# Performance work log

Hardware: AMD Instinct MI355X
Metric: run time of the kernel (lower is better)

## Reference

```python
import jax, jax.numpy as jnp
import numpy as np

DIM = 1024
HIDDEN = 2048
NUM_EXPERTS = 8
TOP_K = 2


def setup_inputs() -> dict:
    key = jax.random.key(0)
    ks = jax.random.split(key, 5)
    x = jax.random.normal(ks[0], (4, 1024, DIM), dtype=jnp.float32)
    # router: torch Linear(dim, num_experts, bias=False) -> store as [dim, E]
    Wr = jax.random.normal(ks[1], (DIM, NUM_EXPERTS), dtype=jnp.float32) * 0.02
    # stacked expert weights (SwiGLU): w1/w3 [E, dim, hidden], w2 [E, hidden, dim]
    W1 = jax.random.normal(ks[2], (NUM_EXPERTS, DIM, HIDDEN), dtype=jnp.float32) * 0.02
    W3 = jax.random.normal(ks[3], (NUM_EXPERTS, DIM, HIDDEN), dtype=jnp.float32) * 0.02
    W2 = jax.random.normal(ks[4], (NUM_EXPERTS, HIDDEN, DIM), dtype=jnp.float32) * 0.02
    return {"x": x, "Wr": Wr, "W1": W1, "W2": W2, "W3": W3}


def reference(x, Wr, W1, W2, W3):
    B, S, D = x.shape
    T = B * S
    xf = x.reshape(T, D)
    # router: softmax over experts, then top-k and renormalize
    probs = jax.nn.softmax(xf @ Wr, axis=-1)                  # [T, E]
    topk_p, topk_i = jax.lax.top_k(probs, TOP_K)              # [T, K]
    topk_p = topk_p / jnp.sum(topk_p, axis=-1, keepdims=True)
    # per-(token, expert) combine weight; zero for non-selected experts
    gate = jnp.sum(jax.nn.one_hot(topk_i, NUM_EXPERTS, dtype=xf.dtype)
                   * topk_p[:, :, None], axis=1)              # [T, E]
    # SwiGLU experts, computed densely then masked-combined (same math as
    # the masked dispatch loop: out[t] = sum_e gate[t,e] * expert_e(x[t]))
    h = jax.nn.silu(jnp.einsum('td,edh->teh', xf, W1)) \
        * jnp.einsum('td,edh->teh', xf, W3)                   # [T, E, H]
    out_e = jnp.einsum('teh,ehd->ted', h, W2)                 # [T, E, D]
    out = jnp.einsum('ted,te->td', out_e, gate)               # [T, D]
    return out.reshape(B, S, D)
```

## Files before the change

### kernel.cpp

```cpp
#include <hip/hip_runtime.h>
#include <hip/hip_bf16.h>
#include <stdint.h>

#define T_TOK 4096
#define DIM   1024
#define HID   2048
#define NE    8

typedef unsigned short ushort_t;
typedef __attribute__((ext_vector_type(8))) short bf16x8;
typedef __attribute__((ext_vector_type(4))) float f32x4;

__device__ __forceinline__ unsigned short f2bf(float f) {
  unsigned u = __float_as_uint(f);
  unsigned r = (u + 0x7fffu + ((u >> 16) & 1u)) >> 16;
  return (unsigned short)r;
}

__device__ __forceinline__ void gl2lds16(const ushort_t* g, ushort_t* l) {
  void* gv = (void*)g;
  __builtin_amdgcn_global_load_lds((__attribute__((address_space(1))) void*)gv,
                                   (__attribute__((address_space(3))) void*)l,
                                   16, 0, 0);
}

__global__ __launch_bounds__(256)
void prep_kernel(const float* __restrict__ x, const float* __restrict__ Wr,
                 const float* __restrict__ W1, const float* __restrict__ W2,
                 const float* __restrict__ W3,
                 ushort_t* __restrict__ xb,
                 ushort_t* __restrict__ w1t, ushort_t* __restrict__ w3t,
                 ushort_t* __restrict__ w2t,
                 int* __restrict__ cnt, int* __restrict__ tok,
                 float* __restrict__ gate, float* __restrict__ out) {
  const int b = blockIdx.x;
  const int tid = threadIdx.x;
  __shared__ float lds[64][65];

  if (b < 12288) {
    const float* src; ushort_t* dst; int R, C, cx, ry;
    const int which = b >> 12;
    const int id = b & 4095;
    const int e = id >> 9, rem = id & 511;
    if (which == 0)      { src = W1; dst = w1t; R = DIM; C = HID; cx = rem & 31; ry = rem >> 5; }
    else if (which == 1) { src = W3; dst = w3t; R = DIM; C = HID; cx = rem & 31; ry = rem >> 5; }
    else                 { src = W2; dst = w2t; R = HID; C = DIM; cx = rem & 15; ry = rem >> 4; }
    const float* s = src + (size_t)e * R * C;
    ushort_t* d = dst + (size_t)e * R * C;
    const int c0 = cx * 64, r0 = ry * 64;
#pragma unroll
    for (int p = 0; p < 4; p++) {
      int idx = p * 256 + tid;
      int r = idx >> 4, c4 = idx & 15;
      float4 v = *(const float4*)(s + (size_t)(r0 + r) * C + c0 + c4 * 4);
      lds[r][c4 * 4 + 0] = v.x; lds[r][c4 * 4 + 1] = v.y;
      lds[r][c4 * 4 + 2] = v.z; lds[r][c4 * 4 + 3] = v.w;
    }
    __syncthreads();
#pragma unroll
    for (int p = 0; p < 4; p++) {
      int idx = p * 256 + tid;
      int cc = idx >> 4, r4 = idx & 15;
      ushort4 o;
      o.x = f2bf(lds[r4 * 4 + 0][cc]);
      o.y = f2bf(lds[r4 * 4 + 1][cc]);
      o.z = f2bf(lds[r4 * 4 + 2][cc]);
      o.w = f2bf(lds[r4 * 4 + 3][cc]);
      *(ushort4*)(d + (size_t)(c0 + cc) * R + r0 + r4 * 4) = o;
    }
  } else if (b < 16384) {
    int i = (b - 12288) * 256 + tid;
    float4 v = ((const float4*)x)[i];
    ushort4 o;
    o.x = f2bf(v.x); o.y = f2bf(v.y); o.z = f2bf(v.z); o.w = f2bf(v.w);
    ((ushort4*)xb)[i] = o;
  } else if (b < 17408) {
    const int wave = tid >> 6;
    const int lane = tid & 63;
    const int t = (b - 16384) * 4 + wave;
    float acc[NE];
#pragma unroll
    for (int e = 0; e < NE; e++) acc[e] = 0.f;
    const float* xr = x + (size_t)t * DIM;
    for (int dd = lane; dd < DIM; dd += 64) {
      float xv = xr[dd];
      const float* wr = Wr + (size_t)dd * NE;
#pragma unroll
      for (int e = 0; e < NE; e++) acc[e] += xv * wr[e];
    }
#pragma unroll
    for (int off = 32; off >= 1; off >>= 1) {
#pragma unroll
      for (int e = 0; e < NE; e++) acc[e] += __shfl_xor(acc[e], off, 64);
    }
    if (lane == 0) {
      int i1 = 0;
#pragma unroll
      for (int e = 1; e < NE; e++) if (acc[e] > acc[i1]) i1 = e;
      int i2 = (i1 == 0) ? 1 : 0;
#pragma unroll
      for (int e = 0; e < NE; e++) {
        if (e == i1) continue;
        if (acc[e] > acc[i2]) i2 = e;
      }
      float r = expf(acc[i2] - acc[i1]);
      float g1 = 1.f / (1.f + r);
      float g2 = 1.f - g1;
      int p;
      p = atomicAdd(&cnt[i1], 1); tok[i1 * T_TOK + p] = t; gate[i1 * T_TOK + p] = g1;
      p = atomicAdd(&cnt[i2], 1); tok[i2 * T_TOK + p] = t; gate[i2 * T_TOK + p] = g2;
    }
  } else {
    int base_i = (b - 17408) * 1024;
    float4 z = {0.f, 0.f, 0.f, 0.f};
#pragma unroll
    for (int it = 0; it < 4; it++) ((float4*)out)[base_i + it * 256 + tid] = z;
  }
}

__global__ __launch_bounds__(256, 3)
void gemm1_kernel(const ushort_t* __restrict__ xb,
                  const ushort_t* __restrict__ w1t,
                  const ushort_t* __restrict__ w3t,
                  const int* __restrict__ tok,
                  const float* __restrict__ gates,
                  const int* __restrict__ cnt,
                  ushort_t* __restrict__ hbuf) {
  const int e = blockIdx.z, mt = blockIdx.y, nt = blockIdx.x;
  const int Ne = cnt[e];
  if (mt * 128 >= Ne) return;
  int be = 0;
#pragma unroll
  for (int i = 0; i < NE; i++) be += (i < e) ? cnt[i] : 0;

  __shared__ __attribute__((aligned(16))) ushort_t lA[128 * 64];
  __shared__ __attribute__((aligned(16))) ushort_t lB1[64 * 64];
  __shared__ __attribute__((aligned(16))) ushort_t lB3[64 * 64];

  const int tid = threadIdx.x, lane = tid & 63, wave = tid >> 6;
  const int kco = ((tid & 7) ^ ((tid >> 3) & 7)) * 8;

  const ushort_t* pA[4];
#pragma unroll
  for (int it = 0; it < 4; it++) {
    int rowg = mt * 128 + it * 32 + (tid >> 3);
    int t = (rowg < Ne) ? tok[e * T_TOK + rowg] : 0;
    pA[it] = xb + (size_t)t * DIM + kco;
  }
  const int h0 = nt * 64;
  const ushort_t* pB1[2];
  const ushort_t* pB3[2];
#pragma unroll
  for (int it = 0; it < 2; it++) {
    int row = h0 + it * 32 + (tid >> 3);
    pB1[it] = w1t + ((size_t)e * HID + row) * DIM + kco;
    pB3[it] = w3t + ((size_t)e * HID + row) * DIM + kco;
  }

  f32x4 c1[4][2], c3[4][2];
#pragma unroll
  for (int i = 0; i < 4; i++)
#pragma unroll
    for (int j = 0; j < 2; j++) {
      c1[i][j] = (f32x4){0.f, 0.f, 0.f, 0.f};
      c3[i][j] = (f32x4){0.f, 0.f, 0.f, 0.f};
    }

  const int wm = (wave >> 1) * 64, wn = (wave & 1) * 32;
  const int m = lane & 15, kq = lane >> 4;
  int aRow[4], bRow[2], cSlot[2];
#pragma unroll
  for (int i = 0; i < 4; i++) aRow[i] = (wm + i * 16 + m) * 64;
#pragma unroll
  for (int j = 0; j < 2; j++) bRow[j] = (wn + j * 16 + m) * 64;
#pragma unroll
  for (int u = 0; u < 2; u++) cSlot[u] = ((u * 4 + kq) ^ (m & 7)) * 8;

  for (int k0 = 0; k0 < DIM; k0 += 64) {
#pragma unroll
    for (int it = 0; it < 4; it++) gl2lds16(pA[it] + k0, lA + (it * 256 + tid) * 8);
#pragma unroll
    for (int it = 0; it < 2; it++) {
      gl2lds16(pB1[it] + k0, lB1 + (it * 256 + tid) * 8);
      gl2lds16(pB3[it] + k0, lB3 + (it * 256 + tid) * 8);
    }
    __syncthreads();
#pragma unroll
    for (int u = 0; u < 2; u++) {
      bf16x8 a[4], b1f[2], b3f[2];
#pragma unroll
      for (int i = 0; i < 4; i++) a[i] = *(const bf16x8*)(lA + aRow[i] + cSlot[u]);
#pragma unroll
      for (int j = 0; j < 2; j++) {
        b1f[j] = *(const bf16x8*)(lB1 + bRow[j] + cSlot[u]);
        b3f[j] = *(const bf16x8*)(lB3 + bRow[j] + cSlot[u]);
      }
#pragma unroll
      for (int i = 0; i < 4; i++)
#pragma unroll
        for (int j = 0; j < 2; j++) {
          c1[i][j] = __builtin_amdgcn_mfma_f32_16x16x32_bf16(a[i], b1f[j], c1[i][j], 0, 0, 0);
          c3[i][j] = __builtin_amdgcn_mfma_f32_16x16x32_bf16(a[i], b3f[j], c3[i][j], 0, 0, 0);
        }
    }
    __syncthreads();
  }

  const int m4 = lane >> 4;
#pragma unroll
  for (int i = 0; i < 4; i++) {
#pragma unroll
    for (int j = 0; j < 2; j++) {
      int hcol = h0 + wn + j * 16 + m;
#pragma unroll
      for (int reg = 0; reg < 4; reg++) {
        int rowg = mt * 128 + wm + i * 16 + m4 * 4 + reg;
        if (rowg < Ne) {
          float v1 = c1[i][j][reg];
          float v3 = c3[i][j][reg];
          float g = gates[e * T_TOK + rowg];
          float hv = g * (v1 / (1.f + expf(-v1))) * v3;
          hbuf[(size_t)(be + rowg) * HID + hcol] = f2bf(hv);
        }
      }
    }
  }
}

__global__ __launch_bounds__(256, 3)
void gemm2_kernel(const ushort_t* __restrict__ hbuf,
                  const ushort_t* __restrict__ w2t,
                  const int* __restrict__ tok,
                  const int* __restrict__ cnt,
                  float* __restrict__ out) {
  const int e = blockIdx.z, mt = blockIdx.y, nt = blockIdx.x;
  const int Ne = cnt[e];
  if (mt * 128 >= Ne) return;
  int be = 0;
#pragma unroll
  for (int i = 0; i < NE; i++) be += (i < e) ? cnt[i] : 0;

  __shared__ __attribute__((aligned(16))) ushort_t lA[128 * 64];
  __shared__ __attribute__((aligned(16))) ushort_t lB[128 * 64];

  const int tid = threadIdx.x, lane = tid & 63, wave = tid >> 6;
  const int kco = ((tid & 7) ^ ((tid >> 3) & 7)) * 8;

  const ushort_t* pA[4];
#pragma unroll
  for (int it = 0; it < 4; it++) {
    int rr = min(mt * 128 + it * 32 + (tid >> 3), Ne - 1);
    pA[it] = hbuf + (size_t)(be + rr) * HID + kco;
  }
  const int d0 = nt * 128;
  const ushort_t* pB[4];
#pragma unroll
  for (int it = 0; it < 4; it++) {
    int row = d0 + it * 32 + (tid >> 3);
    pB[it] = w2t + ((size_t)e * DIM + row) * HID + kco;
  }

  f32x4 c[4][4];
#pragma unroll
  for (int i = 0; i < 4; i++)
#pragma unroll
    for (int j = 0; j < 4; j++) c[i][j] = (f32x4){0.f, 0.f, 0.f, 0.f};

  const int wm = (wave >> 1) * 64, wn = (wave & 1) * 64;
  const int m = lane & 15, kq = lane >> 4;
  int aRow[4], bRow[4], cSlot[2];
#pragma unroll
  for (int i = 0; i < 4; i++) aRow[i] = (wm + i * 16 + m) * 64;
#pragma unroll
  for (int j = 0; j < 4; j++) bRow[j] = (wn + j * 16 + m) * 64;
#pragma unroll
  for (int u = 0; u < 2; u++) cSlot[u] = ((u * 4 + kq) ^ (m & 7)) * 8;

  for (int k0 = 0; k0 < HID; k0 += 64) {
#pragma unroll
    for (int it = 0; it < 4; it++) {
      gl2lds16(pA[it] + k0, lA + (it * 256 + tid) * 8);
      gl2lds16(pB[it] + k0, lB + (it * 256 + tid) * 8);
    }
    __syncthreads();
#pragma unroll
    for (int u = 0; u < 2; u++) {
      bf16x8 a[4], bf[4];
#pragma unroll
      for (int i = 0; i < 4; i++) a[i] = *(const bf16x8*)(lA + aRow[i] + cSlot[u]);
#pragma unroll
      for (int j = 0; j < 4; j++) bf[j] = *(const bf16x8*)(lB + bRow[j] + cSlot[u]);
#pragma unroll
      for (int i = 0; i < 4; i++)
#pragma unroll
        for (int j = 0; j < 4; j++)
          c[i][j] = __builtin_amdgcn_mfma_f32_16x16x32_bf16(a[i], bf[j], c[i][j], 0, 0, 0);
    }
    __syncthreads();
  }

  const int m4 = lane >> 4;
#pragma unroll
  for (int i = 0; i < 4; i++) {
    int rowg = mt * 128 + wm + i * 16 + m4 * 4;
    if (rowg >= Ne) continue;
#pragma unroll
    for (int reg = 0; reg < 4; reg++) {
      int rg = rowg + reg;
      if (rg < Ne) {
        int t = tok[e * T_TOK + rg];
        float* orow = out + (size_t)t * DIM;
#pragma unroll
        for (int j = 0; j < 4; j++) {
          int dcol = d0 + wn + j * 16 + m;
          atomicAdd(orow + dcol, c[i][j][reg]);
        }
      }
    }
  }
}

extern "C" void kernel_launch(void* const* d_in, const int* in_sizes, int n_in,
                              void* d_out, int out_size, void* d_ws, size_t ws_size,
                              hipStream_t stream) {
  (void)in_sizes; (void)n_in; (void)ws_size; (void)out_size;
  const float* x  = (const float*)d_in[0];
  const float* Wr = (const float*)d_in[1];
  const float* W1 = (const float*)d_in[2];
  const float* W2 = (const float*)d_in[3];
  const float* W3 = (const float*)d_in[4];
  float* out = (float*)d_out;

  char* w = (char*)d_ws;
  ushort_t* xb   = (ushort_t*)w; w += (size_t)T_TOK * DIM * 2;
  ushort_t* w1t  = (ushort_t*)w; w += (size_t)NE * DIM * HID * 2;
  ushort_t* w3t  = (ushort_t*)w; w += (size_t)NE * DIM * HID * 2;
  ushort_t* w2t  = (ushort_t*)w; w += (size_t)NE * HID * DIM * 2;
  ushort_t* hbuf = (ushort_t*)w; w += (size_t)2 * T_TOK * HID * 2;
  int*   tok   = (int*)w;   w += (size_t)NE * T_TOK * 4;
  float* gates = (float*)w; w += (size_t)NE * T_TOK * 4;
  int*   cnt   = (int*)w;   w += 128;

  hipMemsetAsync(cnt, 0, 128, stream);
  prep_kernel<<<18432, 256, 0, stream>>>(x, Wr, W1, W2, W3, xb, w1t, w3t, w2t,
                                         cnt, tok, gates, out);
  gemm1_kernel<<<dim3(HID / 64, 32, NE), 256, 0, stream>>>(xb, w1t, w3t, tok, gates, cnt, hbuf);
  gemm2_kernel<<<dim3(DIM / 128, 32, NE), 256, 0, stream>>>(hbuf, w2t, tok, cnt, out);
}
```

Measured before the change: 485.6 us.

## Fuse bf16 cast of x into router pass and move expert dispatch to compact kernel

The router blocks now read each token row once as float4, writing the bf16 copy of x and accumulating the router logits in the same loop. This removes the separate cast-blocks pass over x. Per-token expert ids and gate pairs are stored, and a new single-block compact kernel builds the per-expert token lists using LDS atomics instead of global atomics. That also drops the hipMemsetAsync, but adds an extra serial kernel launch with only one workgroup.

```diff
diff --git a/kernel.cpp b/kernel.cpp
--- a/kernel.cpp
+++ b/kernel.cpp
@@ -31,8 +31,8 @@
                  ushort_t* __restrict__ xb,
                  ushort_t* __restrict__ w1t, ushort_t* __restrict__ w3t,
                  ushort_t* __restrict__ w2t,
-                 int* __restrict__ cnt, int* __restrict__ tok,
-                 float* __restrict__ gate, float* __restrict__ out) {
+                 int* __restrict__ eidx, float2* __restrict__ gpair,
+                 float* __restrict__ out) {
   const int b = blockIdx.x;
   const int tid = threadIdx.x;
   __shared__ float lds[64][65];
@@ -68,25 +68,28 @@
       o.w = f2bf(lds[r4 * 4 + 3][cc]);
       *(ushort4*)(d + (size_t)(c0 + cc) * R + r0 + r4 * 4) = o;
     }
-  } else if (b < 16384) {
-    int i = (b - 12288) * 256 + tid;
-    float4 v = ((const float4*)x)[i];
-    ushort4 o;
-    o.x = f2bf(v.x); o.y = f2bf(v.y); o.z = f2bf(v.z); o.w = f2bf(v.w);
-    ((ushort4*)xb)[i] = o;
-  } else if (b < 17408) {
+  } else if (b < 13312) {
     const int wave = tid >> 6;
     const int lane = tid & 63;
-    const int t = (b - 16384) * 4 + wave;
+    const int t = (b - 12288) * 4 + wave;
+    const float* xr = x + (size_t)t * DIM;
+    ushort_t* xbr = xb + (size_t)t * DIM;
     float acc[NE];
 #pragma unroll
     for (int e = 0; e < NE; e++) acc[e] = 0.f;
-    const float* xr = x + (size_t)t * DIM;
-    for (int dd = lane; dd < DIM; dd += 64) {
-      float xv = xr[dd];
-      const float* wr = Wr + (size_t)dd * NE;
-#pragma unroll
-      for (int e = 0; e < NE; e++) acc[e] += xv * wr[e];
+#pragma unroll
+    for (int it = 0; it < 4; it++) {
+      int d4 = it * 64 + lane;
+      float4 v = ((const float4*)xr)[d4];
+      ushort4 o;
+      o.x = f2bf(v.x); o.y = f2bf(v.y); o.z = f2bf(v.z); o.w = f2bf(v.w);
+      ((ushort4*)xbr)[d4] = o;
+      const float* wr = Wr + (size_t)d4 * 4 * NE;
+      float c[4] = {v.x, v.y, v.z, v.w};
+#pragma unroll
+      for (int cc = 0; cc < 4; cc++)
+#pragma unroll
+        for (int e = 0; e < NE; e++) acc[e] += c[cc] * wr[cc * NE + e];
     }
 #pragma unroll
     for (int off = 32; off >= 1; off >>= 1) {
@@ -105,17 +108,36 @@
       }
       float r = expf(acc[i2] - acc[i1]);
       float g1 = 1.f / (1.f + r);
-      float g2 = 1.f - g1;
-      int p;
-      p = atomicAdd(&cnt[i1], 1); tok[i1 * T_TOK + p] = t; gate[i1 * T_TOK + p] = g1;
-      p = atomicAdd(&cnt[i2], 1); tok[i2 * T_TOK + p] = t; gate[i2 * T_TOK + p] = g2;
+      eidx[t] = i1 | (i2 << 8);
+      gpair[t] = make_float2(g1, 1.f - g1);
     }
   } else {
-    int base_i = (b - 17408) * 1024;
+    int base_i = (b - 13312) * 1024;
     float4 z = {0.f, 0.f, 0.f, 0.f};
 #pragma unroll
     for (int it = 0; it < 4; it++) ((float4*)out)[base_i + it * 256 + tid] = z;
   }
+}
+
+__global__ __launch_bounds__(1024)
+void compact_kernel(const int* __restrict__ eidx, const float2* __restrict__ gpair,
+                    int* __restrict__ cnt, int* __restrict__ tok,
+                    float* __restrict__ gate) {
+  __shared__ int lcnt[NE];
+  const int tid = threadIdx.x;
+  if (tid < NE) lcnt[tid] = 0;
+  __syncthreads();
+  for (int t = tid; t < T_TOK; t += 1024) {
+    int pk = eidx[t];
+    int i1 = pk & 0xff, i2 = (pk >> 8) & 0xff;
+    float2 g = gpair[t];
+    int p1 = atomicAdd(&lcnt[i1], 1);
+    tok[i1 * T_TOK + p1] = t; gate[i1 * T_TOK + p1] = g.x;
+    int p2 = atomicAdd(&lcnt[i2], 1);
+    tok[i2 * T_TOK + p2] = t; gate[i2 * T_TOK + p2] = g.y;
+  }
+  __syncthreads();
+  if (tid < NE) cnt[tid] = lcnt[tid];
 }
 
 __global__ __launch_bounds__(256, 3)
@@ -337,13 +359,15 @@
   ushort_t* w3t  = (ushort_t*)w; w += (size_t)NE * DIM * HID * 2;
   ushort_t* w2t  = (ushort_t*)w; w += (size_t)NE * HID * DIM * 2;
   ushort_t* hbuf = (ushort_t*)w; w += (size_t)2 * T_TOK * HID * 2;
-  int*   tok   = (int*)w;   w += (size_t)NE * T_TOK * 4;
-  float* gates = (float*)w; w += (size_t)NE * T_TOK * 4;
-  int*   cnt   = (int*)w;   w += 128;
-
-  hipMemsetAsync(cnt, 0, 128, stream);
-  prep_kernel<<<18432, 256, 0, stream>>>(x, Wr, W1, W2, W3, xb, w1t, w3t, w2t,
-                                         cnt, tok, gates, out);
+  int*    tok   = (int*)w;    w += (size_t)NE * T_TOK * 4;
+  float*  gates = (float*)w;  w += (size_t)NE * T_TOK * 4;
+  int*    eidx  = (int*)w;    w += (size_t)T_TOK * 4;
+  float2* gpair = (float2*)w; w += (size_t)T_TOK * 8;
+  int*    cnt   = (int*)w;    w += 128;
+
+  prep_kernel<<<14336, 256, 0, stream>>>(x, Wr, W1, W2, W3, xb, w1t, w3t, w2t,
+                                         eidx, gpair, out);
+  compact_kernel<<<1, 1024, 0, stream>>>(eidx, gpair, cnt, tok, gates);
   gemm1_kernel<<<dim3(HID / 64, 32, NE), 256, 0, stream>>>(xb, w1t, w3t, tok, gates, cnt, hbuf);
   gemm2_kernel<<<dim3(DIM / 128, 32, NE), 256, 0, stream>>>(hbuf, w2t, tok, cnt, out);
 }
```

New measurement: 414.0 us. 14.7% less time.
